# Optimization experiments

Hardware: AMD Instinct MI355X
Metric: run time of the kernel (lower is better)

## Reference

```python
import jax, jax.numpy as jnp
import numpy as np


def _cayley():
    """8x8x8 structure constants of Cl(3,0): (a*b)[r] = sum_pq a[p] b[q] C[p,q,r].
    Built by evaluating the original geometric_product formulas on basis one-hots."""
    C = np.zeros((8, 8, 8), dtype=np.float32)
    for p in range(8):
        a = np.zeros(8, dtype=np.float32); a[p] = 1.0
        for q in range(8):
            b = np.zeros(8, dtype=np.float32); b[q] = 1.0
            C[p, q] = [
                a[0]*b[0] + a[1]*b[1] + a[2]*b[2] + a[3]*b[3] - a[4]*b[4] - a[5]*b[5] - a[6]*b[6] - a[7]*b[7],
                a[0]*b[1] + a[1]*b[0] - a[2]*b[4] - a[3]*b[5] + a[4]*b[2] + a[5]*b[3] - a[6]*b[7] - a[7]*b[6],
                a[0]*b[2] + a[1]*b[4] + a[2]*b[0] - a[3]*b[6] - a[4]*b[1] + a[5]*b[7] + a[6]*b[3] + a[7]*b[5],
                a[0]*b[3] + a[1]*b[5] + a[2]*b[6] + a[3]*b[0] - a[4]*b[7] - a[5]*b[1] - a[6]*b[2] - a[7]*b[4],
                a[0]*b[4] + a[1]*b[2] - a[2]*b[1] + a[3]*b[7] + a[4]*b[0] - a[5]*b[6] + a[6]*b[5] + a[7]*b[3],
                a[0]*b[5] + a[1]*b[3] - a[2]*b[7] - a[3]*b[1] + a[4]*b[6] + a[5]*b[0] - a[6]*b[4] - a[7]*b[2],
                a[0]*b[6] + a[1]*b[7] + a[2]*b[3] - a[3]*b[2] - a[4]*b[5] + a[5]*b[4] + a[6]*b[0] + a[7]*b[1],
                a[0]*b[7] + a[1]*b[6] - a[2]*b[5] + a[3]*b[4] + a[4]*b[3] - a[5]*b[2] + a[6]*b[1] + a[7]*b[0],
            ]
    return C

_C = jnp.asarray(_cayley())  # [8,8,8]

BATCH, IN_F, OUT_F = 4096, 512, 512


def setup_inputs() -> dict:
    key = jax.random.key(0)
    k1, k2, k3 = jax.random.split(key, 3)
    return {
        "x": jax.random.normal(k1, (BATCH, IN_F, 8), dtype=jnp.float32),
        "weight": jax.random.normal(k2, (OUT_F, IN_F, 8), dtype=jnp.float32),
        "bias": jax.random.normal(k3, (OUT_F, 8), dtype=jnp.float32),
    }


def reference(x, weight, bias):
    # Precontract weight with Cayley table: Wc[i,j,p,r] = sum_q weight[i,j,q] C[p,q,r]
    Wc = jnp.einsum('ijq,pqr->ijpr', weight, _C)
    # out[b,i,r] = sum_{j,p} x[b,j,p] Wc[i,j,p,r]  (one big GEMM) + bias
    out = jnp.einsum('bjp,ijpr->bir', x, Wc) + bias[None, :, :]
    return out
```

## Files before the change

### kernel.cpp

```cpp
#include <hip/hip_runtime.h>
#include <hip/hip_bf16.h>


#define MDIM 4096
#define NDIM 4096
#define KDIM 4096
#define KTILES 64

typedef __attribute__((ext_vector_type(8))) __bf16 bf16x8;
typedef __attribute__((ext_vector_type(4))) float f32x4;
typedef __attribute__((ext_vector_type(8))) unsigned short ushort8;

__device__ __forceinline__ unsigned short f2bf(float f) {
  unsigned int u = __builtin_bit_cast(unsigned int, f);
  u += 0x7fffu + ((u >> 16) & 1u);
  return (unsigned short)(u >> 16);
}

static constexpr int QTAB[8][8] = {
  {0,1,2,3,4,5,6,7},
  {1,0,4,5,2,3,7,6},
  {2,4,0,6,1,7,3,5},
  {3,5,6,0,7,1,2,4},
  {4,2,1,7,0,6,5,3},
  {5,3,7,1,6,0,4,2},
  {6,7,3,2,5,4,0,1},
  {7,6,5,4,3,2,1,0},
};
static constexpr unsigned short SBIT[8][8] = {
  {0,0,0,0,0x8000,0x8000,0x8000,0x8000},
  {0,0,0x8000,0x8000,0,0,0x8000,0x8000},
  {0,0,0,0x8000,0x8000,0,0,0},
  {0,0,0,0,0x8000,0x8000,0x8000,0x8000},
  {0,0,0x8000,0,0,0x8000,0,0},
  {0,0,0x8000,0x8000,0,0,0x8000,0x8000},
  {0,0,0,0x8000,0x8000,0,0,0},
  {0,0,0x8000,0,0,0x8000,0,0},
};

__global__ __launch_bounds__(256) void cast_x_kernel(
    const float* __restrict__ X, unsigned short* __restrict__ Xb) {
  const size_t t = (size_t)blockIdx.x * 256 + threadIdx.x;
  const float4* p = (const float4*)(X + t * 8);
  float4 a = p[0], b = p[1];
  ushort8 o;
  o[0] = f2bf(a.x); o[1] = f2bf(a.y); o[2] = f2bf(a.z); o[3] = f2bf(a.w);
  o[4] = f2bf(b.x); o[5] = f2bf(b.y); o[6] = f2bf(b.z); o[7] = f2bf(b.w);
  *(ushort8*)(Xb + t * 8) = o;
}

__global__ __launch_bounds__(256) void build_wc_kernel(
    const float* __restrict__ W, unsigned short* __restrict__ Wb) {
  const int t = blockIdx.x * 256 + threadIdx.x;
  const int i = t >> 9;
  const int j = t & 511;
  const float4 w0 = *(const float4*)(W + (size_t)t * 8);
  const float4 w1 = *(const float4*)(W + (size_t)t * 8 + 4);
  const unsigned short b[8] = {f2bf(w0.x), f2bf(w0.y), f2bf(w0.z), f2bf(w0.w),
                               f2bf(w1.x), f2bf(w1.y), f2bf(w1.z), f2bf(w1.w)};
#pragma unroll
  for (int r = 0; r < 8; ++r) {
    ushort8 o;
#pragma unroll
    for (int p = 0; p < 8; ++p)
      o[p] = (unsigned short)(b[QTAB[r][p]] ^ SBIT[r][p]);
    *(ushort8*)(Wb + (size_t)(i * 8 + r) * KDIM + j * 8) = o;
  }
}

typedef const __attribute__((address_space(1))) unsigned int as1_uint;
typedef __attribute__((address_space(3))) unsigned int as3_uint;

__device__ __forceinline__ void gload_lds16(const unsigned short* g,
                                            unsigned short* l) {
  __builtin_amdgcn_global_load_lds((as1_uint*)g, (as3_uint*)l, 16, 0, 0);
}

__device__ __forceinline__ void stage_half(
    const unsigned short* __restrict__ G, int gbase_row, int tile, int kh,
    unsigned short* lds_slot, int wid, int lane) {
  const int colswz = ((lane & 3) ^ ((lane >> 3) & 3)) * 8;
#pragma unroll
  for (int q = 0; q < 2; ++q) {
    const int c = wid * 2 + q;
    const unsigned short* src = G
        + (size_t)(gbase_row + c * 16 + (lane >> 2)) * KDIM
        + tile * 64 + kh * 32 + colswz;
    gload_lds16(src, lds_slot + c * 512);
  }
}

#define BAR()  asm volatile("s_barrier" ::: "memory")
#define VM6()  asm volatile("s_waitcnt vmcnt(6)" ::: "memory")
#define VM0()  asm volatile("s_waitcnt vmcnt(0)" ::: "memory")

#define RDA(dst, bufb, kk, mh) do {                                           \
    _Pragma("unroll") for (int mi_ = 0; mi_ < 4; ++mi_)                       \
      dst[mi_] = *(const bf16x8*)(&lds[(bufb)*4 + (kk)][0]                    \
          + ((wm)*128 + ((mh)*4 + mi_)*16 + fr)*32 + fqs*8);                  \
  } while (0)
#define RDB_(dst, bufb, kk) do {                                              \
    _Pragma("unroll") for (int ni_ = 0; ni_ < 4; ++ni_)                       \
      dst[ni_] = *(const bf16x8*)(&lds[(bufb)*4 + 2 + (kk)][0]                \
          + ((wn)*64 + ni_*16 + fr)*32 + fqs*8);                              \
  } while (0)
#define MFMA16(afv, bv, mh) do {                                              \
    __builtin_amdgcn_s_setprio(1);                                            \
    _Pragma("unroll") for (int mi_ = 0; mi_ < 4; ++mi_) {                     \
      _Pragma("unroll") for (int ni_ = 0; ni_ < 4; ++ni_)                     \
        acc[(mh)*4 + mi_][ni_] = __builtin_amdgcn_mfma_f32_16x16x32_bf16(     \
            afv[mi_], bv[ni_], acc[(mh)*4 + mi_][ni_], 0, 0, 0);              \
    }                                                                         \
    __builtin_amdgcn_s_setprio(0);                                            \
  } while (0)

__global__ __launch_bounds__(512, 2) void gemm_bt_bias(
    const unsigned short* __restrict__ A,
    const unsigned short* __restrict__ B,
    const float* __restrict__ bias,
    float* __restrict__ C) {
  __shared__ unsigned short lds[8][8192];

  const int tid = threadIdx.x;
  const int wid = tid >> 6;
  const int lane = tid & 63;
  const int wm = wid >> 2;
  const int wn = wid & 3;
  const int fr = lane & 15;
  const int fq = lane >> 4;
  const int fqs = fq ^ ((fr >> 1) & 3);

  const int raw = blockIdx.x;
  const int wg = (raw & 7) * 32 + (raw >> 3);
  const int brow = (wg >> 4) * 256;
  const int bcol = (wg & 15) * 256;

  f32x4 acc[8][4];
#pragma unroll
  for (int m = 0; m < 8; ++m)
#pragma unroll
    for (int n = 0; n < 4; ++n) acc[m][n] = (f32x4){0.f, 0.f, 0.f, 0.f};
  bf16x8 afA[4], afB[4], bU[4], bV[4];

  stage_half(A, brow, 0, 0, &lds[0][0], wid, lane);
  stage_half(A, brow, 0, 1, &lds[1][0], wid, lane);
  stage_half(B, bcol, 0, 0, &lds[2][0], wid, lane);
  stage_half(B, bcol, 0, 1, &lds[3][0], wid, lane);
  stage_half(A, brow, 1, 0, &lds[4][0], wid, lane);
  stage_half(B, bcol, 1, 0, &lds[6][0], wid, lane);
  stage_half(B, bcol, 1, 1, &lds[7][0], wid, lane);
  VM6();
  BAR();
  RDA(afA, 0, 0, 0);
  RDB_(bU, 0, 0);

  for (int i = 0; i < KTILES / 2 - 1; ++i) {
    const int t0 = 2 * i, t1 = 2 * i + 1;
    stage_half(A, brow, t1, 1, &lds[5][0], wid, lane);
    BAR(); RDA(afB, 0, 0, 1);                  MFMA16(afA, bU, 0); BAR();
    stage_half(B, bcol, t0 + 2, 0, &lds[2][0], wid, lane);
    BAR(); RDA(afA, 0, 1, 0); RDB_(bV, 0, 1);  MFMA16(afB, bU, 1); BAR();
    stage_half(A, brow, t0 + 2, 0, &lds[0][0], wid, lane);
    BAR(); RDA(afB, 0, 1, 1);                  MFMA16(afA, bV, 0); BAR();
    stage_half(B, bcol, t0 + 2, 1, &lds[3][0], wid, lane);
    VM6();
    BAR(); RDA(afA, 1, 0, 0); RDB_(bU, 1, 0);  MFMA16(afB, bV, 1); BAR();
    stage_half(A, brow, t0 + 2, 1, &lds[1][0], wid, lane);
    BAR(); RDA(afB, 1, 0, 1);                  MFMA16(afA, bU, 0); BAR();
    stage_half(B, bcol, t1 + 2, 0, &lds[6][0], wid, lane);
    BAR(); RDA(afA, 1, 1, 0); RDB_(bV, 1, 1);  MFMA16(afB, bU, 1); BAR();
    stage_half(A, brow, t1 + 2, 0, &lds[4][0], wid, lane);
    BAR(); RDA(afB, 1, 1, 1);                  MFMA16(afA, bV, 0); BAR();
    stage_half(B, bcol, t1 + 2, 1, &lds[7][0], wid, lane);
    VM6();
    BAR(); RDA(afA, 0, 0, 0); RDB_(bU, 0, 0);  MFMA16(afB, bV, 1); BAR();
  }

  stage_half(A, brow, KTILES - 1, 1, &lds[5][0], wid, lane);
  BAR(); RDA(afB, 0, 0, 1);                  MFMA16(afA, bU, 0); BAR();
  BAR(); RDA(afA, 0, 1, 0); RDB_(bV, 0, 1);  MFMA16(afB, bU, 1); BAR();
  BAR(); RDA(afB, 0, 1, 1);                  MFMA16(afA, bV, 0); BAR();
  VM0();
  BAR(); RDA(afA, 1, 0, 0); RDB_(bU, 1, 0);  MFMA16(afB, bV, 1); BAR();
  BAR(); RDA(afB, 1, 0, 1);                  MFMA16(afA, bU, 0); BAR();
  BAR(); RDA(afA, 1, 1, 0); RDB_(bV, 1, 1);  MFMA16(afB, bU, 1); BAR();
  BAR(); RDA(afB, 1, 1, 1);                  MFMA16(afA, bV, 0); BAR();
  BAR();                                     MFMA16(afB, bV, 1); BAR();

#pragma unroll
  for (int n = 0; n < 4; ++n) {
    const int col = bcol + wn * 64 + n * 16 + fr;
    const float bvs = bias[col];
#pragma unroll
    for (int m = 0; m < 8; ++m) {
      const int row0 = brow + wm * 128 + m * 16 + fq * 4;
#pragma unroll
      for (int j = 0; j < 4; ++j)
        C[(size_t)(row0 + j) * NDIM + col] = acc[m][n][j] + bvs;
    }
  }
}

extern "C" void kernel_launch(void* const* d_in, const int* in_sizes, int n_in,
                              void* d_out, int out_size, void* d_ws, size_t ws_size,
                              hipStream_t stream) {
  const float* x = (const float*)d_in[0];
  const float* w = (const float*)d_in[1];
  const float* bias = (const float*)d_in[2];
  float* out = (float*)d_out;

  unsigned short* Xb = (unsigned short*)d_ws;
  unsigned short* Wb = Xb + (size_t)MDIM * KDIM;

  cast_x_kernel<<<8192, 256, 0, stream>>>(x, Xb);
  build_wc_kernel<<<1024, 256, 0, stream>>>(w, Wb);
  gemm_bt_bias<<<256, 512, 0, stream>>>(Xb, Wb, bias, out);
}
```

Before: 250.8 us.

## Restructure GEMM main loop to one barrier per step with finer-grained staging

The main K loop is reorganised so each sub-step issues one half-tile async load, an optional vmcnt wait, a single barrier, then LDS reads and MFMAs. The previous version used two barriers per sub-step. The prologue stages fewer halves, and the B-tile loads for the next tile are interleaved with the A loads. The goal is to cut barrier stalls and spread global-to-LDS traffic more evenly over the loop. The risk is LDS write-after-read hazards with only one barrier per step, and shorter prefetch distance for some halves.

```diff
diff --git a/kernel.cpp b/kernel.cpp
--- a/kernel.cpp
+++ b/kernel.cpp
@@ -92,7 +92,9 @@
 
 #define BAR()  asm volatile("s_barrier" ::: "memory")
 #define VM6()  asm volatile("s_waitcnt vmcnt(6)" ::: "memory")
+#define VM4()  asm volatile("s_waitcnt vmcnt(4)" ::: "memory")
 #define VM0()  asm volatile("s_waitcnt vmcnt(0)" ::: "memory")
+#define NOP_() (void)0
 
 #define RDA(dst, bufb, kk, mh) do {                                           \
     _Pragma("unroll") for (int mi_ = 0; mi_ < 4; ++mi_)                       \
@@ -114,6 +116,14 @@
     __builtin_amdgcn_s_setprio(0);                                            \
   } while (0)
 
+#define BLK(STAGE_STMT, VM_STMT, READ_STMT, afv, bv, mh) do {                 \
+    STAGE_STMT;                                                               \
+    VM_STMT;                                                                  \
+    BAR();                                                                    \
+    READ_STMT;                                                                \
+    MFMA16(afv, bv, mh);                                                      \
+  } while (0)
+
 __global__ __launch_bounds__(512, 2) void gemm_bt_bias(
     const unsigned short* __restrict__ A,
     const unsigned short* __restrict__ B,
@@ -143,49 +153,50 @@
   bf16x8 afA[4], afB[4], bU[4], bV[4];
 
   stage_half(A, brow, 0, 0, &lds[0][0], wid, lane);
+  stage_half(B, bcol, 0, 0, &lds[2][0], wid, lane);
   stage_half(A, brow, 0, 1, &lds[1][0], wid, lane);
-  stage_half(B, bcol, 0, 0, &lds[2][0], wid, lane);
   stage_half(B, bcol, 0, 1, &lds[3][0], wid, lane);
   stage_half(A, brow, 1, 0, &lds[4][0], wid, lane);
-  stage_half(B, bcol, 1, 0, &lds[6][0], wid, lane);
-  stage_half(B, bcol, 1, 1, &lds[7][0], wid, lane);
   VM6();
   BAR();
   RDA(afA, 0, 0, 0);
   RDB_(bU, 0, 0);
 
   for (int i = 0; i < KTILES / 2 - 1; ++i) {
-    const int t0 = 2 * i, t1 = 2 * i + 1;
-    stage_half(A, brow, t1, 1, &lds[5][0], wid, lane);
-    BAR(); RDA(afB, 0, 0, 1);                  MFMA16(afA, bU, 0); BAR();
-    stage_half(B, bcol, t0 + 2, 0, &lds[2][0], wid, lane);
-    BAR(); RDA(afA, 0, 1, 0); RDB_(bV, 0, 1);  MFMA16(afB, bU, 1); BAR();
-    stage_half(A, brow, t0 + 2, 0, &lds[0][0], wid, lane);
-    BAR(); RDA(afB, 0, 1, 1);                  MFMA16(afA, bV, 0); BAR();
-    stage_half(B, bcol, t0 + 2, 1, &lds[3][0], wid, lane);
-    VM6();
-    BAR(); RDA(afA, 1, 0, 0); RDB_(bU, 1, 0);  MFMA16(afB, bV, 1); BAR();
-    stage_half(A, brow, t0 + 2, 1, &lds[1][0], wid, lane);
-    BAR(); RDA(afB, 1, 0, 1);                  MFMA16(afA, bU, 0); BAR();
-    stage_half(B, bcol, t1 + 2, 0, &lds[6][0], wid, lane);
-    BAR(); RDA(afA, 1, 1, 0); RDB_(bV, 1, 1);  MFMA16(afB, bU, 1); BAR();
-    stage_half(A, brow, t1 + 2, 0, &lds[4][0], wid, lane);
-    BAR(); RDA(afB, 1, 1, 1);                  MFMA16(afA, bV, 0); BAR();
-    stage_half(B, bcol, t1 + 2, 1, &lds[7][0], wid, lane);
-    VM6();
-    BAR(); RDA(afA, 0, 0, 0); RDB_(bU, 0, 0);  MFMA16(afB, bV, 1); BAR();
-  }
-
-  stage_half(A, brow, KTILES - 1, 1, &lds[5][0], wid, lane);
-  BAR(); RDA(afB, 0, 0, 1);                  MFMA16(afA, bU, 0); BAR();
-  BAR(); RDA(afA, 0, 1, 0); RDB_(bV, 0, 1);  MFMA16(afB, bU, 1); BAR();
-  BAR(); RDA(afB, 0, 1, 1);                  MFMA16(afA, bV, 0); BAR();
-  VM0();
-  BAR(); RDA(afA, 1, 0, 0); RDB_(bU, 1, 0);  MFMA16(afB, bV, 1); BAR();
-  BAR(); RDA(afB, 1, 0, 1);                  MFMA16(afA, bU, 0); BAR();
-  BAR(); RDA(afA, 1, 1, 0); RDB_(bV, 1, 1);  MFMA16(afB, bU, 1); BAR();
-  BAR(); RDA(afB, 1, 1, 1);                  MFMA16(afA, bV, 0); BAR();
-  BAR();                                     MFMA16(afB, bV, 1); BAR();
+    const int t1 = 2 * i + 1, tn0 = 2 * i + 2, tn1 = 2 * i + 3;
+    BLK(stage_half(B, bcol, t1, 0, &lds[6][0], wid, lane), NOP_(),
+        RDA(afB, 0, 0, 1),                    afA, bU, 0);
+    BLK(stage_half(A, brow, t1, 1, &lds[5][0], wid, lane), VM6(),
+        { RDA(afA, 0, 1, 0); RDB_(bV, 0, 1); }, afB, bU, 1);
+    BLK(stage_half(B, bcol, t1, 1, &lds[7][0], wid, lane), NOP_(),
+        RDA(afB, 0, 1, 1),                    afA, bV, 0);
+    BLK(stage_half(A, brow, tn0, 0, &lds[0][0], wid, lane), VM6(),
+        { RDA(afA, 1, 0, 0); RDB_(bU, 1, 0); }, afB, bV, 1);
+    BLK(stage_half(B, bcol, tn0, 0, &lds[2][0], wid, lane), NOP_(),
+        RDA(afB, 1, 0, 1),                    afA, bU, 0);
+    BLK(stage_half(A, brow, tn0, 1, &lds[1][0], wid, lane), VM6(),
+        { RDA(afA, 1, 1, 0); RDB_(bV, 1, 1); }, afB, bU, 1);
+    BLK(stage_half(B, bcol, tn0, 1, &lds[3][0], wid, lane), NOP_(),
+        RDA(afB, 1, 1, 1),                    afA, bV, 0);
+    BLK(stage_half(A, brow, tn1, 0, &lds[4][0], wid, lane), VM6(),
+        { RDA(afA, 0, 0, 0); RDB_(bU, 0, 0); }, afB, bV, 1);
+  }
+
+  BLK(stage_half(B, bcol, KTILES - 1, 0, &lds[6][0], wid, lane), NOP_(),
+      RDA(afB, 0, 0, 1),                    afA, bU, 0);
+  BLK(stage_half(A, brow, KTILES - 1, 1, &lds[5][0], wid, lane), VM6(),
+      { RDA(afA, 0, 1, 0); RDB_(bV, 0, 1); }, afB, bU, 1);
+  BLK(stage_half(B, bcol, KTILES - 1, 1, &lds[7][0], wid, lane), NOP_(),
+      RDA(afB, 0, 1, 1),                    afA, bV, 0);
+  BLK(NOP_(), VM4(),
+      { RDA(afA, 1, 0, 0); RDB_(bU, 1, 0); }, afB, bV, 1);
+  BLK(NOP_(), NOP_(),
+      RDA(afB, 1, 0, 1),                    afA, bU, 0);
+  BLK(NOP_(), VM0(),
+      { RDA(afA, 1, 1, 0); RDB_(bV, 1, 1); }, afB, bU, 1);
+  BLK(NOP_(), NOP_(),
+      RDA(afB, 1, 1, 1),                    afA, bV, 0);
+  BLK(NOP_(), NOP_(), NOP_(),               afB, bV, 1);
 
 #pragma unroll
   for (int n = 0; n < 4; ++n) {
```

After: 238.2 us. -5.0%, faster.
